# Optimization experiments

Hardware: AMD Instinct MI355X
Metric: run time of the kernel (lower is better)

## Reference

```python
import jax, jax.numpy as jnp
import numpy as np

LRELU_ALPHA = 0.2   # LeakyReLU negative slope (alpha init arg)
NEG_INF = -9e15     # masking constant used by standard GAT layers

B, N, NFEAT, NHID, NHEAD, NPRED = 16, 1024, 16, 32, 4, 12


def setup_inputs() -> dict:
    key = jax.random.key(0)
    ks = jax.random.split(key, 8)
    x = jax.random.normal(ks[0], (B, N, NFEAT), dtype=jnp.float32)
    adj = jax.random.randint(ks[1], (N, N), 0, 2, dtype=jnp.int32)
    s = 0.1
    W = jax.random.normal(ks[2], (NHEAD, NFEAT, NHID), dtype=jnp.float32) * s
    a_src = jax.random.normal(ks[3], (NHEAD, NHID), dtype=jnp.float32) * s
    a_dst = jax.random.normal(ks[4], (NHEAD, NHID), dtype=jnp.float32) * s
    W_out = jax.random.normal(ks[5], (NHEAD * NHID, NPRED), dtype=jnp.float32) * s
    a_out_src = jax.random.normal(ks[6], (NPRED,), dtype=jnp.float32) * s
    a_out_dst = jax.random.normal(ks[7], (NPRED,), dtype=jnp.float32) * s
    return {"x": x, "adj": adj, "W": W, "a_src": a_src, "a_dst": a_dst,
            "W_out": W_out, "a_out_src": a_out_src, "a_out_dst": a_out_dst}


def reference(x, adj, W, a_src, a_dst, W_out, a_out_src, a_out_dst):
    # Eval mode: all F.dropout calls are identity.
    mask = adj > 0  # [N, N], broadcast over batch (and heads)

    # --- multi-head GAT layer (concat=True), all heads vectorized ---
    Wh = jnp.einsum('bnf,hfk->bhnk', x, W)                 # [B,H,N,K]
    f_src = jnp.einsum('bhnk,hk->bhn', Wh, a_src)          # [B,H,N]
    f_dst = jnp.einsum('bhnk,hk->bhn', Wh, a_dst)
    e = jax.nn.leaky_relu(f_src[..., :, None] + f_dst[..., None, :], LRELU_ALPHA)
    attn = jax.nn.softmax(jnp.where(mask, e, NEG_INF), axis=-1)  # [B,H,N,N]
    h = jax.nn.elu(jnp.einsum('bhnm,bhmk->bhnk', attn, Wh))      # concat=True -> ELU
    b, H, n, k = h.shape
    h = jnp.transpose(h, (0, 2, 1, 3)).reshape(b, n, H * k)  # concat heads, dim=2

    # --- output GAT layer (concat=False) ---
    Wh2 = h @ W_out                                        # [B,N,npred]
    g_src = Wh2 @ a_out_src                                # [B,N]
    g_dst = Wh2 @ a_out_dst
    e2 = jax.nn.leaky_relu(g_src[:, :, None] + g_dst[:, None, :], LRELU_ALPHA)
    attn2 = jax.nn.softmax(jnp.where(mask, e2, NEG_INF), axis=-1)
    out = jax.nn.elu(jnp.einsum('bnm,bmp->bnp', attn2, Wh2))  # outer F.elu in STGAT
    return out.reshape(b, -1)                              # [B, N*npred]
```

## Files before the change

### kernel.cpp

```cpp
#include <hip/hip_runtime.h>
#include <cmath>

#define B_    16
#define N_    1024
#define NHID_ 32
#define NHEAD_ 4
#define NPRED_ 12
#define ALPHA 0.2f
#define LOG2E 1.442695041f

typedef __attribute__((ext_vector_type(8)))  short          short8;
typedef __attribute__((ext_vector_type(4)))  float          floatx4;
typedef __attribute__((ext_vector_type(2)))  float          float2v;
typedef __attribute__((ext_vector_type(4)))  unsigned       uintx4;
typedef __attribute__((ext_vector_type(4)))  unsigned short ushort4v;
typedef __attribute__((ext_vector_type(8)))  unsigned short ushort8v;

__device__ __forceinline__ float bs2f(unsigned short s) {
    return __uint_as_float(((unsigned)s) << 16);
}
__device__ __forceinline__ short f2bs(float f) {
    unsigned u = __float_as_uint(f);
    unsigned r = (u + 0x7fffu + ((u >> 16) & 1u)) >> 16;
    return (short)r;
}
__device__ __forceinline__ float ldin(const void* p, long i, int isbf) {
    if (isbf) return bs2f(((const unsigned short*)p)[i]);
    return ((const float*)p)[i];
}
__device__ __forceinline__ float fexp2(float x) {
#if __has_builtin(__builtin_amdgcn_exp2f)
    return __builtin_amdgcn_exp2f(x);
#else
    return __expf(x * 0.6931471805599453f);
#endif
}
__device__ __forceinline__ unsigned pk2t(unsigned u0, unsigned u1) {
#if __has_builtin(__builtin_amdgcn_perm)
    return __builtin_amdgcn_perm(u1, u0, 0x07060302u);
#else
    return (u0 >> 16) | (u1 & 0xffff0000u);
#endif
}
__device__ __forceinline__ float2v vmax2(float2v a, float2v b) {
#if __has_builtin(__builtin_elementwise_max)
    return __builtin_elementwise_max(a, b);
#else
    float2v r; r.x = fmaxf(a.x, b.x); r.y = fmaxf(a.y, b.y); return r;
#endif
}
__device__ __forceinline__ float2v vfma2(float2v a, float2v b, float2v c) {
#if __has_builtin(__builtin_elementwise_fma)
    return __builtin_elementwise_fma(a, b, c);
#else
    float2v r; r.x = __builtin_fmaf(a.x, b.x, c.x); r.y = __builtin_fmaf(a.y, b.y, c.y); return r;
#endif
}
__device__ __forceinline__ int detect_isbf(const unsigned short* xu) {
    int lane = threadIdx.x & 63;
    uint4 v = ((const uint4*)xu)[lane];
    unsigned wv[4] = {v.x, v.y, v.z, v.w};
    bool any = false;
#pragma unroll
    for (int i = 0; i < 4; ++i) {
        any |= (((wv[i] & 0xffffu) >> 7) & 0xffu) >= 160u;
        any |= (((wv[i] >> 16) >> 7) & 0xffu) >= 160u;
    }
    return __popcll(__ballot(any)) < 8;
}

__global__ __launch_bounds__(256) void k01_prep_wh(
    const unsigned short* __restrict__ xu, const int* __restrict__ adj,
    const void* __restrict__ x, const void* __restrict__ W,
    const void* __restrict__ a_src, const void* __restrict__ a_dst,
    unsigned short* __restrict__ bias,
    short* __restrict__ WhB, float* __restrict__ f_src, float* __restrict__ f_dst)
{
    int tid = threadIdx.x;
    if (blockIdx.x < 512) {
        int gid = blockIdx.x * 256 + tid;
        long base = (long)gid * 8;
        int4 a0 = *(const int4*)(adj + base);
        int4 a1 = *(const int4*)(adj + base + 4);
        uint4 wv;
        wv.x = (a0.x ? 0u : 0xFF80u) | (a0.y ? 0u : 0xFF800000u);
        wv.y = (a0.z ? 0u : 0xFF80u) | (a0.w ? 0u : 0xFF800000u);
        wv.z = (a1.x ? 0u : 0xFF80u) | (a1.y ? 0u : 0xFF800000u);
        wv.w = (a1.z ? 0u : 0xFF80u) | (a1.w ? 0u : 0xFF800000u);
        *(uint4*)(bias + base) = wv;
        return;
    }
    int isbf = detect_isbf(xu);
    __shared__ float Ws[16][32];
    __shared__ float xs[32][17];
    __shared__ float as_s[32], ad_s[32];
    __shared__ float Wa_s[16], Wad_s[16];
    int bid = blockIdx.x - 512;
    int bh = bid >> 5;
    int n0 = (bid & 31) * 32;
    int b  = bh >> 2, hh = bh & 3;

    if (!isbf) {
        const float* Wf = (const float*)W + hh * 512;
        if (tid < 128) {
            float4 v = *(const float4*)(Wf + tid * 4);
            int f = (tid * 4) >> 5, k = (tid * 4) & 31;
            Ws[f][k] = v.x; Ws[f][k+1] = v.y; Ws[f][k+2] = v.z; Ws[f][k+3] = v.w;
        }
        const float* xf = (const float*)x + ((long)(b * N_ + n0)) * 16;
        if (tid < 128) {
            float4 v = *(const float4*)(xf + tid * 4);
            int r = tid >> 2, f = (tid & 3) * 4;
            xs[r][f] = v.x; xs[r][f+1] = v.y; xs[r][f+2] = v.z; xs[r][f+3] = v.w;
        }
    } else {
        const unsigned short* Wb = (const unsigned short*)W + hh * 512;
        if (tid < 128) {
            ushort4v v = *(const ushort4v*)(Wb + tid * 4);
            int f = (tid * 4) >> 5, k = (tid * 4) & 31;
            Ws[f][k] = bs2f(v[0]); Ws[f][k+1] = bs2f(v[1]);
            Ws[f][k+2] = bs2f(v[2]); Ws[f][k+3] = bs2f(v[3]);
        }
        const unsigned short* xb = (const unsigned short*)x + ((long)(b * N_ + n0)) * 16;
        if (tid < 64) {
            ushort8v v = *(const ushort8v*)(xb + tid * 8);
            int r = tid >> 1, f = (tid & 1) * 8;
#pragma unroll
            for (int i = 0; i < 8; ++i) xs[r][f + i] = bs2f(v[i]);
        }
    }
    if (tid < 32) {
        as_s[tid] = ldin(a_src, hh * 32 + tid, isbf);
        ad_s[tid] = ldin(a_dst, hh * 32 + tid, isbf);
    }
    __syncthreads();

    if (tid < 32) {
        int f = tid & 15;
        const float* av = (tid < 16) ? as_s : ad_s;
        float s = 0.f;
#pragma unroll
        for (int kk = 0; kk < 32; ++kk) s += Ws[f][kk] * av[kk];
        ((tid < 16) ? Wa_s : Wad_s)[f] = s;
    }
    __syncthreads();

    if (tid < 32) {
        float fs = 0.f, fd = 0.f;
#pragma unroll
        for (int f = 0; f < 16; ++f) {
            fs += xs[tid][f] * Wa_s[f];
            fd += xs[tid][f] * Wad_s[f];
        }
        int n = n0 + tid;
        f_src[bh * N_ + n] = fs * LOG2E;
        f_dst[bh * N_ + n] = fd * LOG2E;
    }

    int k = tid & 31, rb = tid >> 5;
#pragma unroll
    for (int it = 0; it < 4; ++it) {
        int r = it * 8 + rb;
        float acc = 0.f;
#pragma unroll
        for (int f = 0; f < 16; ++f) acc += xs[r][f] * Ws[f][k];
        int n = n0 + r;
        int kstep = n >> 5, quad = (n >> 3) & 3, jj = n & 7;
        int t = k >> 4, l = quad * 16 + (k & 15);
        WhB[((((size_t)bh * 32 + kstep) * 2 + t) * 64 + l) * 8 + jj] = f2bs(acc);
    }
}

__global__ __launch_bounds__(256) void k2_attn1(
    const float* __restrict__ f_src, const float* __restrict__ f_dst,
    const unsigned short* __restrict__ bias, const short* __restrict__ WhB,
    unsigned short* __restrict__ h2)
{
    __shared__ float fdst_s[N_];
    __shared__ float wmax[4];
    __shared__ float Sh[2][2][16];
    __shared__ float xch[2][64][8];
    int bid = blockIdx.x;
    int xcd = bid & 7, j = bid >> 3;
    int bh = j & 63;
    int tile = xcd + 8 * (j >> 6);
    int tid = threadIdx.x;
    int w = tid >> 6, lane = tid & 63;
    int rh = w & 1, ch = w >> 1;

    float lmax = -INFINITY;
    for (int idx = tid; idx < N_; idx += 256) {
        float v = f_dst[bh * N_ + idx];
        fdst_s[idx] = v;
        lmax = fmaxf(lmax, v);
    }
#pragma unroll
    for (int m = 32; m; m >>= 1) lmax = fmaxf(lmax, __shfl_xor(lmax, m, 64));
    if (lane == 0) wmax[w] = lmax;
    __syncthreads();
    float maxfd = fmaxf(fmaxf(wmax[0], wmax[1]), fmaxf(wmax[2], wmax[3]));

    int i0 = tile * 32 + rh * 16;
    int r = lane & 15, q = lane >> 4;

    float fsr = f_src[bh * N_ + i0 + r];
    float Mv = fsr + maxfd;
    float M = fmaxf(Mv, ALPHA * Mv);
    float2v a1v; a1v.x = fsr - M;          a1v.y = a1v.x;
    float2v a2v; a2v.x = ALPHA * fsr - M;  a2v.y = a2v.x;
    float2v alv; alv.x = ALPHA;            alv.y = ALPHA;
    float2v s2 = {};

    floatx4 acc0 = {}, acc1 = {};
    const unsigned short* brow = bias + (size_t)(i0 + r) * N_ + ch * 512 + q * 8;
    const float* fdp = fdst_s + ch * 512 + q * 8;

    uint4  bu_n = *(const uint4*)(brow);
    float4 fa_n = *(const float4*)(fdp);
    float4 fb_n = *(const float4*)(fdp + 4);

#pragma unroll 4
    for (int kk = 0; kk < 16; ++kk) {
        uint4 bu = bu_n; float4 fda = fa_n; float4 fdb = fb_n;
        if (kk < 15) {
            bu_n = *(const uint4*)(brow + (kk + 1) * 32);
            fa_n = *(const float4*)(fdp + (kk + 1) * 32);
            fb_n = *(const float4*)(fdp + (kk + 1) * 32 + 4);
        }
        unsigned bw[4] = {bu.x, bu.y, bu.z, bu.w};
        float fdx[8] = {fda.x, fda.y, fda.z, fda.w, fdb.x, fdb.y, fdb.z, fdb.w};
        unsigned dpk[4];
#pragma unroll
        for (int p = 0; p < 4; ++p) {
            float2v fd2; fd2.x = fdx[2 * p]; fd2.y = fdx[2 * p + 1];
            float2v b2;  b2.x = __uint_as_float(bw[p] << 16);
                         b2.y = __uint_as_float(bw[p] & 0xffff0000u);
            float2v t1 = a1v + fd2;
            float2v t2 = vfma2(alv, fd2, a2v);
            float2v arg = vmax2(t1, t2) + b2;
            float2v pv; pv.x = fexp2(arg.x); pv.y = fexp2(arg.y);
            s2 += pv;
            dpk[p] = pk2t(__float_as_uint(pv.x), __float_as_uint(pv.y));
        }
        uintx4 du; du[0] = dpk[0]; du[1] = dpk[1]; du[2] = dpk[2]; du[3] = dpk[3];
        short8 afr = __builtin_bit_cast(short8, du);
        const short* bbase = WhB + ((((size_t)bh * 32 + ch * 16 + kk) * 2) * 64 + lane) * 8;
        short8 bfr0 = *(const short8*)(bbase);
        short8 bfr1 = *(const short8*)(bbase + 512);
        acc0 = __builtin_amdgcn_mfma_f32_16x16x32_bf16(afr, bfr0, acc0, 0, 0, 0);
        acc1 = __builtin_amdgcn_mfma_f32_16x16x32_bf16(afr, bfr1, acc1, 0, 0, 0);
    }

    float s = s2.x + s2.y;
    s += __shfl_xor(s, 16, 64);
    s += __shfl_xor(s, 32, 64);
    if (lane < 16) Sh[rh][ch][lane] = s;
    if (ch == 1) {
#pragma unroll
        for (int i = 0; i < 4; ++i) {
            xch[rh][lane][i]     = acc0[i];
            xch[rh][lane][4 + i] = acc1[i];
        }
    }
    __syncthreads();
    if (ch == 0) {
#pragma unroll
        for (int i = 0; i < 4; ++i) {
            acc0[i] += xch[rh][lane][i];
            acc1[i] += xch[rh][lane][4 + i];
        }
        int bb = bh >> 2, head = bh & 3;
#pragma unroll
        for (int reg = 0; reg < 4; ++reg) {
            int row = q * 4 + reg;
            float rsv = 1.f / (Sh[rh][0][row] + Sh[rh][1][row]);
            unsigned short* hrow = &h2[((size_t)(bb * N_ + i0 + row)) * 128 + head * 32];
            float v0 = acc0[reg] * rsv;
            v0 = v0 > 0.f ? v0 : expm1f(v0);
            hrow[r]      = (unsigned short)f2bs(v0);
            float v1 = acc1[reg] * rsv;
            v1 = v1 > 0.f ? v1 : expm1f(v1);
            hrow[16 + r] = (unsigned short)f2bs(v1);
        }
    }
}

__global__ __launch_bounds__(256) void k3_out_proj(
    const unsigned short* __restrict__ xu,
    const unsigned short* __restrict__ h2, const void* __restrict__ W_out,
    const void* __restrict__ a_out_src, const void* __restrict__ a_out_dst,
    short* __restrict__ Wh2B, float* __restrict__ g_src, float* __restrict__ g_dst)
{
    int isbf = detect_isbf(xu);
    __shared__ float WoT[16][132];
    __shared__ float hs[16][132];
    __shared__ float aos[16], aod[16];
    int bid = blockIdx.x;
    int b = bid >> 6;
    int n0 = (bid & 63) * 16;
    int tid = threadIdx.x;

    if (!isbf) {
        const float* Wf = (const float*)W_out;
        for (int idx = tid; idx < 384; idx += 256) {
            float4 v = *(const float4*)(Wf + idx * 4);
            float vv[4] = {v.x, v.y, v.z, v.w};
#pragma unroll
            for (int i = 0; i < 4; ++i) {
                int e = idx * 4 + i;
                WoT[e % NPRED_][e / NPRED_] = vv[i];
            }
        }
    } else {
        const unsigned short* Wb = (const unsigned short*)W_out;
        for (int idx = tid; idx < 192; idx += 256) {
            ushort8v v = *(const ushort8v*)(Wb + idx * 8);
#pragma unroll
            for (int i = 0; i < 8; ++i) {
                int e = idx * 8 + i;
                WoT[e % NPRED_][e / NPRED_] = bs2f(v[i]);
            }
        }
    }
    if (tid < 128) {
#pragma unroll
        for (int p = NPRED_; p < 16; ++p) WoT[p][tid] = 0.f;
    }
    if (tid < 16) {
        aos[tid] = (tid < NPRED_) ? ldin(a_out_src, tid, isbf) : 0.f;
        aod[tid] = (tid < NPRED_) ? ldin(a_out_dst, tid, isbf) : 0.f;
    }
    {
        ushort8v v = *(const ushort8v*)(h2 + ((size_t)(b * N_ + n0 + (tid >> 4))) * 128 + (tid & 15) * 8);
        int r = tid >> 4, c8 = (tid & 15) * 8;
#pragma unroll
        for (int i = 0; i < 8; ++i) hs[r][c8 + i] = bs2f(v[i]);
    }
    __syncthreads();

    int r = tid >> 4, p = tid & 15;
    float acc = 0.f;
#pragma unroll 8
    for (int c4 = 0; c4 < 128; c4 += 4) {
        float4 hv = *(const float4*)&hs[r][c4];
        float4 wv = *(const float4*)&WoT[p][c4];
        acc += hv.x * wv.x + hv.y * wv.y + hv.z * wv.z + hv.w * wv.w;
    }

    float t1 = acc * aos[p], t2 = acc * aod[p];
#pragma unroll
    for (int m = 8; m; m >>= 1) {
        t1 += __shfl_xor(t1, m, 64);
        t2 += __shfl_xor(t2, m, 64);
    }
    int n = n0 + r;
    if (p == 0) {
        g_src[b * N_ + n] = t1 * LOG2E;
        g_dst[b * N_ + n] = t2 * LOG2E;
    }
    int kstep = n >> 5, quad = (n >> 3) & 3, jj = n & 7;
    short val = (p == 15) ? (short)0x3F80 : f2bs(acc);
    Wh2B[(((size_t)b * 32 + kstep) * 64 + quad * 16 + p) * 8 + jj] = val;
}

__global__ __launch_bounds__(256) void k4_attn2(
    const unsigned short* __restrict__ xu,
    const float* __restrict__ g_src, const float* __restrict__ g_dst,
    const unsigned short* __restrict__ bias, const short* __restrict__ Wh2B,
    void* __restrict__ out)
{
    int isbf = detect_isbf(xu);
    __shared__ float gdst_s[N_];
    __shared__ float wmax[4];
    __shared__ float xch[3][64][4];
    int bid = blockIdx.x;
    int xcd = bid & 7, j = bid >> 3;
    int b = j & 15;
    int tile = xcd + 8 * (j >> 4);
    int tid = threadIdx.x;
    int ch = tid >> 6, lane = tid & 63;

    float lmax = -INFINITY;
    for (int idx = tid; idx < N_; idx += 256) {
        float v = g_dst[b * N_ + idx];
        gdst_s[idx] = v;
        lmax = fmaxf(lmax, v);
    }
#pragma unroll
    for (int m = 32; m; m >>= 1) lmax = fmaxf(lmax, __shfl_xor(lmax, m, 64));
    if (lane == 0) wmax[ch] = lmax;
    __syncthreads();
    float maxgd = fmaxf(fmaxf(wmax[0], wmax[1]), fmaxf(wmax[2], wmax[3]));

    int i0 = tile * 16;
    int r = lane & 15, q = lane >> 4;

    float gsr = g_src[b * N_ + i0 + r];
    float Mv = gsr + maxgd;
    float M = fmaxf(Mv, ALPHA * Mv);
    float2v a1v; a1v.x = gsr - M;          a1v.y = a1v.x;
    float2v a2v; a2v.x = ALPHA * gsr - M;  a2v.y = a2v.x;
    float2v alv; alv.x = ALPHA;            alv.y = ALPHA;

    floatx4 acc = {};
    const unsigned short* brow = bias + (size_t)(i0 + r) * N_ + ch * 256 + q * 8;
    const float* fdp = gdst_s + ch * 256 + q * 8;

    uint4  bu_n = *(const uint4*)(brow);
    float4 fa_n = *(const float4*)(fdp);
    float4 fb_n = *(const float4*)(fdp + 4);

#pragma unroll 4
    for (int kk = 0; kk < 8; ++kk) {
        uint4 bu = bu_n; float4 fda = fa_n; float4 fdb = fb_n;
        if (kk < 7) {
            bu_n = *(const uint4*)(brow + (kk + 1) * 32);
            fa_n = *(const float4*)(fdp + (kk + 1) * 32);
            fb_n = *(const float4*)(fdp + (kk + 1) * 32 + 4);
        }
        unsigned bw[4] = {bu.x, bu.y, bu.z, bu.w};
        float fdx[8] = {fda.x, fda.y, fda.z, fda.w, fdb.x, fdb.y, fdb.z, fdb.w};
        unsigned dpk[4];
#pragma unroll
        for (int p = 0; p < 4; ++p) {
            float2v fd2; fd2.x = fdx[2 * p]; fd2.y = fdx[2 * p + 1];
            float2v b2;  b2.x = __uint_as_float(bw[p] << 16);
                         b2.y = __uint_as_float(bw[p] & 0xffff0000u);
            float2v t1 = a1v + fd2;
            float2v t2 = vfma2(alv, fd2, a2v);
            float2v arg = vmax2(t1, t2) + b2;
            float2v pv; pv.x = fexp2(arg.x); pv.y = fexp2(arg.y);
            dpk[p] = pk2t(__float_as_uint(pv.x), __float_as_uint(pv.y));
        }
        uintx4 du; du[0] = dpk[0]; du[1] = dpk[1]; du[2] = dpk[2]; du[3] = dpk[3];
        short8 afr = __builtin_bit_cast(short8, du);
        short8 bfr = *(const short8*)(Wh2B + (((size_t)b * 32 + ch * 8 + kk) * 64 + lane) * 8);
        acc = __builtin_amdgcn_mfma_f32_16x16x32_bf16(afr, bfr, acc, 0, 0, 0);
    }

    if (ch != 0) {
#pragma unroll
        for (int i = 0; i < 4; ++i) xch[ch - 1][lane][i] = acc[i];
    }
    __syncthreads();
    if (ch == 0) {
#pragma unroll
        for (int t = 0; t < 3; ++t)
#pragma unroll
            for (int i = 0; i < 4; ++i) acc[i] += xch[t][lane][i];
        int srclane = (lane & 48) + 15;
#pragma unroll
        for (int reg = 0; reg < 4; ++reg) {
            int row = q * 4 + reg;
            float Srow = __shfl(acc[reg], srclane, 64);
            float v = acc[reg] / Srow;
            float o = v > 0.f ? v : expm1f(v);
            if (r < NPRED_) {
                size_t idx = (size_t)b * (N_ * NPRED_) + (size_t)(i0 + row) * NPRED_ + r;
                if (isbf) ((unsigned short*)out)[idx] = (unsigned short)f2bs(o);
                else      ((float*)out)[idx] = o;
            }
        }
    }
}

extern "C" void kernel_launch(void* const* d_in, const int* in_sizes, int n_in,
                              void* d_out, int out_size, void* d_ws, size_t ws_size,
                              hipStream_t stream)
{
    (void)in_sizes; (void)n_in; (void)out_size; (void)ws_size;
    const void* x      = d_in[0];
    const int*  adj    = (const int*)d_in[1];
    const void* W      = d_in[2];
    const void* a_src  = d_in[3];
    const void* a_dst  = d_in[4];
    const void* W_out  = d_in[5];
    const void* a_osrc = d_in[6];
    const void* a_odst = d_in[7];
    const unsigned short* xu = (const unsigned short*)x;

    char* ws = (char*)d_ws;
    short* WhB   = (short*)(ws);
    float* f_src = (float*)(ws + (4 << 20));
    float* f_dst = (float*)(ws + (4 << 20) + (256 << 10));
    unsigned short* h2 = (unsigned short*)(ws + (4 << 20) + (512 << 10));
    short* Wh2B  = (short*)(ws + (12 << 20) + (512 << 10));
    float* g_src = (float*)(ws + (13 << 20));
    float* g_dst = (float*)(ws + (13 << 20) + (64 << 10));
    unsigned short* bias = (unsigned short*)(ws + (14 << 20));

    hipLaunchKernelGGL(k01_prep_wh, dim3(2560), dim3(256), 0, stream,
                       xu, adj, x, W, a_src, a_dst, bias, WhB, f_src, f_dst);
    hipLaunchKernelGGL(k2_attn1,    dim3(2048), dim3(256), 0, stream,
                       f_src, f_dst, bias, WhB, h2);
    hipLaunchKernelGGL(k3_out_proj, dim3(1024), dim3(256), 0, stream,
                       xu, h2, W_out, a_osrc, a_odst, Wh2B, g_src, g_dst);
    hipLaunchKernelGGL(k4_attn2,    dim3(1024), dim3(256), 0, stream,
                       xu, g_src, g_dst, bias, Wh2B, d_out);
}
```

Measured before the change: 120.0 us.

## Stage bias tile in padded LDS and split attention K-range across four waves

Both attention kernels now cooperatively copy the 16-row bias tile into a padded shared-memory buffer with coalesced 16-byte loads, instead of each lane streaming its own strided global bias reads. k2 is restructured so each block handles 16 rows with four waves splitting the key dimension (a 4-way reduction of partial sums and accumulators), and the grid doubles to cover it. The Wh B-fragment loads are now software-prefetched one iteration ahead instead of the bias loads. This adds about 33KB of LDS per block, which may reduce occupancy, and adds a larger cross-wave reduction.

```diff
diff --git a/kernel.cpp b/kernel.cpp
--- a/kernel.cpp
+++ b/kernel.cpp
@@ -8,11 +8,13 @@
 #define NPRED_ 12
 #define ALPHA 0.2f
 #define LOG2E 1.442695041f
+#define BP    1044
 
 typedef __attribute__((ext_vector_type(8)))  short          short8;
 typedef __attribute__((ext_vector_type(4)))  float          floatx4;
 typedef __attribute__((ext_vector_type(2)))  float          float2v;
 typedef __attribute__((ext_vector_type(4)))  unsigned       uintx4;
+typedef __attribute__((ext_vector_type(2)))  unsigned       uintx2;
 typedef __attribute__((ext_vector_type(4)))  unsigned short ushort4v;
 typedef __attribute__((ext_vector_type(8)))  unsigned short ushort8v;
 
@@ -177,16 +179,17 @@
     unsigned short* __restrict__ h2)
 {
     __shared__ float fdst_s[N_];
+    __shared__ __align__(16) unsigned short bias_s[16 * BP];
     __shared__ float wmax[4];
-    __shared__ float Sh[2][2][16];
-    __shared__ float xch[2][64][8];
+    __shared__ float Sh[4][16];
+    __shared__ float xch[3][64][8];
     int bid = blockIdx.x;
     int xcd = bid & 7, j = bid >> 3;
     int bh = j & 63;
     int tile = xcd + 8 * (j >> 6);
     int tid = threadIdx.x;
-    int w = tid >> 6, lane = tid & 63;
-    int rh = w & 1, ch = w >> 1;
+    int ch = tid >> 6, lane = tid & 63;
+    int i0 = tile * 16;
 
     float lmax = -INFINITY;
     for (int idx = tid; idx < N_; idx += 256) {
@@ -196,11 +199,23 @@
     }
 #pragma unroll
     for (int m = 32; m; m >>= 1) lmax = fmaxf(lmax, __shfl_xor(lmax, m, 64));
-    if (lane == 0) wmax[w] = lmax;
+    if (lane == 0) wmax[ch] = lmax;
+
+    {
+        const unsigned short* gsrc = bias + (size_t)i0 * N_;
+#pragma unroll
+        for (int it = 0; it < 8; ++it) {
+            int e = (it * 256 + tid) * 8;
+            ushort8v v = *(const ushort8v*)(gsrc + e);
+            int rr = e >> 10, cc = e & 1023;
+            unsigned short* d = &bias_s[rr * BP + cc];
+            *(ushort4v*)d = __builtin_shufflevector(v, v, 0, 1, 2, 3);
+            *(ushort4v*)(d + 4) = __builtin_shufflevector(v, v, 4, 5, 6, 7);
+        }
+    }
     __syncthreads();
     float maxfd = fmaxf(fmaxf(wmax[0], wmax[1]), fmaxf(wmax[2], wmax[3]));
 
-    int i0 = tile * 32 + rh * 16;
     int r = lane & 15, q = lane >> 4;
 
     float fsr = f_src[bh * N_ + i0 + r];
@@ -212,22 +227,27 @@
     float2v s2 = {};
 
     floatx4 acc0 = {}, acc1 = {};
-    const unsigned short* brow = bias + (size_t)(i0 + r) * N_ + ch * 512 + q * 8;
-    const float* fdp = fdst_s + ch * 512 + q * 8;
-
-    uint4  bu_n = *(const uint4*)(brow);
-    float4 fa_n = *(const float4*)(fdp);
-    float4 fb_n = *(const float4*)(fdp + 4);
-
-#pragma unroll 4
-    for (int kk = 0; kk < 16; ++kk) {
-        uint4 bu = bu_n; float4 fda = fa_n; float4 fdb = fb_n;
-        if (kk < 15) {
-            bu_n = *(const uint4*)(brow + (kk + 1) * 32);
-            fa_n = *(const float4*)(fdp + (kk + 1) * 32);
-            fb_n = *(const float4*)(fdp + (kk + 1) * 32 + 4);
-        }
-        unsigned bw[4] = {bu.x, bu.y, bu.z, bu.w};
+    const unsigned short* bls = bias_s + r * BP + ch * 256 + q * 8;
+    const float* fdp = fdst_s + ch * 256 + q * 8;
+    const short* wb = WhB + ((((size_t)bh * 32 + ch * 8) * 2) * 64 + lane) * 8;
+
+    short8 w0_n = *(const short8*)(wb);
+    short8 w1_n = *(const short8*)(wb + 512);
+
+#pragma unroll
+    for (int kk = 0; kk < 8; ++kk) {
+        short8 bfr0 = w0_n, bfr1 = w1_n;
+        if (kk < 7) {
+            w0_n = *(const short8*)(wb + (kk + 1) * 1024);
+            w1_n = *(const short8*)(wb + (kk + 1) * 1024 + 512);
+        }
+        ushort4v blo = *(const ushort4v*)(bls + kk * 32);
+        ushort4v bhi = *(const ushort4v*)(bls + kk * 32 + 4);
+        uintx2 u0 = __builtin_bit_cast(uintx2, blo);
+        uintx2 u1 = __builtin_bit_cast(uintx2, bhi);
+        unsigned bw[4] = {u0[0], u0[1], u1[0], u1[1]};
+        float4 fda = *(const float4*)(fdp + kk * 32);
+        float4 fdb = *(const float4*)(fdp + kk * 32 + 4);
         float fdx[8] = {fda.x, fda.y, fda.z, fda.w, fdb.x, fdb.y, fdb.z, fdb.w};
         unsigned dpk[4];
 #pragma unroll
@@ -244,9 +264,6 @@
         }
         uintx4 du; du[0] = dpk[0]; du[1] = dpk[1]; du[2] = dpk[2]; du[3] = dpk[3];
         short8 afr = __builtin_bit_cast(short8, du);
-        const short* bbase = WhB + ((((size_t)bh * 32 + ch * 16 + kk) * 2) * 64 + lane) * 8;
-        short8 bfr0 = *(const short8*)(bbase);
-        short8 bfr1 = *(const short8*)(bbase + 512);
         acc0 = __builtin_amdgcn_mfma_f32_16x16x32_bf16(afr, bfr0, acc0, 0, 0, 0);
         acc1 = __builtin_amdgcn_mfma_f32_16x16x32_bf16(afr, bfr1, acc1, 0, 0, 0);
     }
@@ -254,26 +271,28 @@
     float s = s2.x + s2.y;
     s += __shfl_xor(s, 16, 64);
     s += __shfl_xor(s, 32, 64);
-    if (lane < 16) Sh[rh][ch][lane] = s;
-    if (ch == 1) {
+    if (lane < 16) Sh[ch][lane] = s;
+    if (ch != 0) {
 #pragma unroll
         for (int i = 0; i < 4; ++i) {
-            xch[rh][lane][i]     = acc0[i];
-            xch[rh][lane][4 + i] = acc1[i];
+            xch[ch - 1][lane][i]     = acc0[i];
+            xch[ch - 1][lane][4 + i] = acc1[i];
         }
     }
     __syncthreads();
     if (ch == 0) {
 #pragma unroll
-        for (int i = 0; i < 4; ++i) {
-            acc0[i] += xch[rh][lane][i];
-            acc1[i] += xch[rh][lane][4 + i];
-        }
+        for (int t = 0; t < 3; ++t)
+#pragma unroll
+            for (int i = 0; i < 4; ++i) {
+                acc0[i] += xch[t][lane][i];
+                acc1[i] += xch[t][lane][4 + i];
+            }
         int bb = bh >> 2, head = bh & 3;
 #pragma unroll
         for (int reg = 0; reg < 4; ++reg) {
             int row = q * 4 + reg;
-            float rsv = 1.f / (Sh[rh][0][row] + Sh[rh][1][row]);
+            float rsv = 1.f / (Sh[0][row] + Sh[1][row] + Sh[2][row] + Sh[3][row]);
             unsigned short* hrow = &h2[((size_t)(bb * N_ + i0 + row)) * 128 + head * 32];
             float v0 = acc0[reg] * rsv;
             v0 = v0 > 0.f ? v0 : expm1f(v0);
@@ -371,6 +390,7 @@
 {
     int isbf = detect_isbf(xu);
     __shared__ float gdst_s[N_];
+    __shared__ __align__(16) unsigned short bias_s[16 * BP];
     __shared__ float wmax[4];
     __shared__ float xch[3][64][4];
     int bid = blockIdx.x;
@@ -379,6 +399,7 @@
     int tile = xcd + 8 * (j >> 4);
     int tid = threadIdx.x;
     int ch = tid >> 6, lane = tid & 63;
+    int i0 = tile * 16;
 
     float lmax = -INFINITY;
     for (int idx = tid; idx < N_; idx += 256) {
@@ -389,10 +410,22 @@
 #pragma unroll
     for (int m = 32; m; m >>= 1) lmax = fmaxf(lmax, __shfl_xor(lmax, m, 64));
     if (lane == 0) wmax[ch] = lmax;
+
+    {
+        const unsigned short* gsrc = bias + (size_t)i0 * N_;
+#pragma unroll
+        for (int it = 0; it < 8; ++it) {
+            int e = (it * 256 + tid) * 8;
+            ushort8v v = *(const ushort8v*)(gsrc + e);
+            int rr = e >> 10, cc = e & 1023;
+            unsigned short* d = &bias_s[rr * BP + cc];
+            *(ushort4v*)d = __builtin_shufflevector(v, v, 0, 1, 2, 3);
+            *(ushort4v*)(d + 4) = __builtin_shufflevector(v, v, 4, 5, 6, 7);
+        }
+    }
     __syncthreads();
     float maxgd = fmaxf(fmaxf(wmax[0], wmax[1]), fmaxf(wmax[2], wmax[3]));
 
-    int i0 = tile * 16;
     int r = lane & 15, q = lane >> 4;
 
     float gsr = g_src[b * N_ + i0 + r];
@@ -403,22 +436,23 @@
     float2v alv; alv.x = ALPHA;            alv.y = ALPHA;
 
     floatx4 acc = {};
-    const unsigned short* brow = bias + (size_t)(i0 + r) * N_ + ch * 256 + q * 8;
+    const unsigned short* bls = bias_s + r * BP + ch * 256 + q * 8;
     const float* fdp = gdst_s + ch * 256 + q * 8;
-
-    uint4  bu_n = *(const uint4*)(brow);
-    float4 fa_n = *(const float4*)(fdp);
-    float4 fb_n = *(const float4*)(fdp + 4);
-
-#pragma unroll 4
+    const short* wb = Wh2B + (((size_t)b * 32 + ch * 8) * 64 + lane) * 8;
+
+    short8 wf_n = *(const short8*)(wb);
+
+#pragma unroll
     for (int kk = 0; kk < 8; ++kk) {
-        uint4 bu = bu_n; float4 fda = fa_n; float4 fdb = fb_n;
-        if (kk < 7) {
-            bu_n = *(const uint4*)(brow + (kk + 1) * 32);
-            fa_n = *(const float4*)(fdp + (kk + 1) * 32);
-            fb_n = *(const float4*)(fdp + (kk + 1) * 32 + 4);
-        }
-        unsigned bw[4] = {bu.x, bu.y, bu.z, bu.w};
+        short8 bfr = wf_n;
+        if (kk < 7) wf_n = *(const short8*)(wb + (kk + 1) * 512);
+        ushort4v blo = *(const ushort4v*)(bls + kk * 32);
+        ushort4v bhi = *(const ushort4v*)(bls + kk * 32 + 4);
+        uintx2 u0 = __builtin_bit_cast(uintx2, blo);
+        uintx2 u1 = __builtin_bit_cast(uintx2, bhi);
+        unsigned bw[4] = {u0[0], u0[1], u1[0], u1[1]};
+        float4 fda = *(const float4*)(fdp + kk * 32);
+        float4 fdb = *(const float4*)(fdp + kk * 32 + 4);
         float fdx[8] = {fda.x, fda.y, fda.z, fda.w, fdb.x, fdb.y, fdb.z, fdb.w};
         unsigned dpk[4];
 #pragma unroll
@@ -434,7 +468,6 @@
         }
         uintx4 du; du[0] = dpk[0]; du[1] = dpk[1]; du[2] = dpk[2]; du[3] = dpk[3];
         short8 afr = __builtin_bit_cast(short8, du);
-        short8 bfr = *(const short8*)(Wh2B + (((size_t)b * 32 + ch * 8 + kk) * 64 + lane) * 8);
         acc = __builtin_amdgcn_mfma_f32_16x16x32_bf16(afr, bfr, acc, 0, 0, 0);
     }
 
@@ -491,7 +524,7 @@
 
     hipLaunchKernelGGL(k01_prep_wh, dim3(2560), dim3(256), 0, stream,
                        xu, adj, x, W, a_src, a_dst, bias, WhB, f_src, f_dst);
-    hipLaunchKernelGGL(k2_attn1,    dim3(2048), dim3(256), 0, stream,
+    hipLaunchKernelGGL(k2_attn1,    dim3(4096), dim3(256), 0, stream,
                        f_src, f_dst, bias, WhB, h2);
     hipLaunchKernelGGL(k3_out_proj, dim3(1024), dim3(256), 0, stream,
                        xu, h2, W_out, a_osrc, a_odst, Wh2B, g_src, g_dst);
```

Measured after the change: 129.0 us. 7.5% more time.

## Give each wave a full key range in attn1 and prefetch MFMA B fragments

Applied to the files above, without the earlier changes.

The first attention kernel now has each of its four waves own 16 query rows across all 1024 keys, so a block covers 64 rows. This drops the split-K cross-wave reduction through shared memory and the block barrier, and halves the grid. Both attention kernels now software-prefetch the Wh B-fragments from global memory one iteration ahead and read the f_dst values from LDS on demand instead of prefetching them. In exchange, each wave runs a longer serial loop and there are fewer blocks to hide latency, while register pressure shifts from the LDS prefetch to the global prefetch.

```diff
diff --git a/kernel.cpp b/kernel.cpp
--- a/kernel.cpp
+++ b/kernel.cpp
@@ -178,15 +178,13 @@
 {
     __shared__ float fdst_s[N_];
     __shared__ float wmax[4];
-    __shared__ float Sh[2][2][16];
-    __shared__ float xch[2][64][8];
+    __shared__ float Sh[4][16];
     int bid = blockIdx.x;
     int xcd = bid & 7, j = bid >> 3;
     int bh = j & 63;
     int tile = xcd + 8 * (j >> 6);
     int tid = threadIdx.x;
     int w = tid >> 6, lane = tid & 63;
-    int rh = w & 1, ch = w >> 1;
 
     float lmax = -INFINITY;
     for (int idx = tid; idx < N_; idx += 256) {
@@ -200,7 +198,7 @@
     __syncthreads();
     float maxfd = fmaxf(fmaxf(wmax[0], wmax[1]), fmaxf(wmax[2], wmax[3]));
 
-    int i0 = tile * 32 + rh * 16;
+    int i0 = tile * 64 + w * 16;
     int r = lane & 15, q = lane >> 4;
 
     float fsr = f_src[bh * N_ + i0 + r];
@@ -212,21 +210,25 @@
     float2v s2 = {};
 
     floatx4 acc0 = {}, acc1 = {};
-    const unsigned short* brow = bias + (size_t)(i0 + r) * N_ + ch * 512 + q * 8;
-    const float* fdp = fdst_s + ch * 512 + q * 8;
+    const unsigned short* brow = bias + (size_t)(i0 + r) * N_ + q * 8;
+    const float* fdp = fdst_s + q * 8;
+    const short* wb = WhB + (((size_t)bh * 64) * 64 + lane) * 8;
 
     uint4  bu_n = *(const uint4*)(brow);
-    float4 fa_n = *(const float4*)(fdp);
-    float4 fb_n = *(const float4*)(fdp + 4);
+    short8 w0_n = *(const short8*)(wb);
+    short8 w1_n = *(const short8*)(wb + 512);
 
 #pragma unroll 4
-    for (int kk = 0; kk < 16; ++kk) {
-        uint4 bu = bu_n; float4 fda = fa_n; float4 fdb = fb_n;
-        if (kk < 15) {
+    for (int kk = 0; kk < 32; ++kk) {
+        uint4 bu = bu_n;
+        short8 bfr0 = w0_n, bfr1 = w1_n;
+        if (kk < 31) {
             bu_n = *(const uint4*)(brow + (kk + 1) * 32);
-            fa_n = *(const float4*)(fdp + (kk + 1) * 32);
-            fb_n = *(const float4*)(fdp + (kk + 1) * 32 + 4);
-        }
+            w0_n = *(const short8*)(wb + (kk + 1) * 1024);
+            w1_n = *(const short8*)(wb + (kk + 1) * 1024 + 512);
+        }
+        float4 fda = *(const float4*)(fdp + kk * 32);
+        float4 fdb = *(const float4*)(fdp + kk * 32 + 4);
         unsigned bw[4] = {bu.x, bu.y, bu.z, bu.w};
         float fdx[8] = {fda.x, fda.y, fda.z, fda.w, fdb.x, fdb.y, fdb.z, fdb.w};
         unsigned dpk[4];
@@ -244,9 +246,6 @@
         }
         uintx4 du; du[0] = dpk[0]; du[1] = dpk[1]; du[2] = dpk[2]; du[3] = dpk[3];
         short8 afr = __builtin_bit_cast(short8, du);
-        const short* bbase = WhB + ((((size_t)bh * 32 + ch * 16 + kk) * 2) * 64 + lane) * 8;
-        short8 bfr0 = *(const short8*)(bbase);
-        short8 bfr1 = *(const short8*)(bbase + 512);
         acc0 = __builtin_amdgcn_mfma_f32_16x16x32_bf16(afr, bfr0, acc0, 0, 0, 0);
         acc1 = __builtin_amdgcn_mfma_f32_16x16x32_bf16(afr, bfr1, acc1, 0, 0, 0);
     }
@@ -254,34 +253,21 @@
     float s = s2.x + s2.y;
     s += __shfl_xor(s, 16, 64);
     s += __shfl_xor(s, 32, 64);
-    if (lane < 16) Sh[rh][ch][lane] = s;
-    if (ch == 1) {
-#pragma unroll
-        for (int i = 0; i < 4; ++i) {
-            xch[rh][lane][i]     = acc0[i];
-            xch[rh][lane][4 + i] = acc1[i];
-        }
-    }
-    __syncthreads();
-    if (ch == 0) {
-#pragma unroll
-        for (int i = 0; i < 4; ++i) {
-            acc0[i] += xch[rh][lane][i];
-            acc1[i] += xch[rh][lane][4 + i];
-        }
-        int bb = bh >> 2, head = bh & 3;
-#pragma unroll
-        for (int reg = 0; reg < 4; ++reg) {
-            int row = q * 4 + reg;
-            float rsv = 1.f / (Sh[rh][0][row] + Sh[rh][1][row]);
-            unsigned short* hrow = &h2[((size_t)(bb * N_ + i0 + row)) * 128 + head * 32];
-            float v0 = acc0[reg] * rsv;
-            v0 = v0 > 0.f ? v0 : expm1f(v0);
-            hrow[r]      = (unsigned short)f2bs(v0);
-            float v1 = acc1[reg] * rsv;
-            v1 = v1 > 0.f ? v1 : expm1f(v1);
-            hrow[16 + r] = (unsigned short)f2bs(v1);
-        }
+    if (lane < 16) Sh[w][lane] = s;
+    __builtin_amdgcn_wave_barrier();
+
+    int bb = bh >> 2, head = bh & 3;
+#pragma unroll
+    for (int reg = 0; reg < 4; ++reg) {
+        int row = q * 4 + reg;
+        float rsv = 1.f / Sh[w][row];
+        unsigned short* hrow = &h2[((size_t)(bb * N_ + i0 + row)) * 128 + head * 32];
+        float v0 = acc0[reg] * rsv;
+        v0 = v0 > 0.f ? v0 : expm1f(v0);
+        hrow[r]      = (unsigned short)f2bs(v0);
+        float v1 = acc1[reg] * rsv;
+        v1 = v1 > 0.f ? v1 : expm1f(v1);
+        hrow[16 + r] = (unsigned short)f2bs(v1);
     }
 }
 
@@ -405,19 +391,21 @@
     floatx4 acc = {};
     const unsigned short* brow = bias + (size_t)(i0 + r) * N_ + ch * 256 + q * 8;
     const float* fdp = gdst_s + ch * 256 + q * 8;
+    const short* wb = Wh2B + (((size_t)b * 32 + ch * 8) * 64 + lane) * 8;
 
     uint4  bu_n = *(const uint4*)(brow);
-    float4 fa_n = *(const float4*)(fdp);
-    float4 fb_n = *(const float4*)(fdp + 4);
+    short8 wf_n = *(const short8*)(wb);
 
 #pragma unroll 4
     for (int kk = 0; kk < 8; ++kk) {
-        uint4 bu = bu_n; float4 fda = fa_n; float4 fdb = fb_n;
+        uint4 bu = bu_n;
+        short8 bfr = wf_n;
         if (kk < 7) {
             bu_n = *(const uint4*)(brow + (kk + 1) * 32);
-            fa_n = *(const float4*)(fdp + (kk + 1) * 32);
-            fb_n = *(const float4*)(fdp + (kk + 1) * 32 + 4);
-        }
+            wf_n = *(const short8*)(wb + (kk + 1) * 512);
+        }
+        float4 fda = *(const float4*)(fdp + kk * 32);
+        float4 fdb = *(const float4*)(fdp + kk * 32 + 4);
         unsigned bw[4] = {bu.x, bu.y, bu.z, bu.w};
         float fdx[8] = {fda.x, fda.y, fda.z, fda.w, fdb.x, fdb.y, fdb.z, fdb.w};
         unsigned dpk[4];
@@ -434,7 +422,6 @@
         }
         uintx4 du; du[0] = dpk[0]; du[1] = dpk[1]; du[2] = dpk[2]; du[3] = dpk[3];
         short8 afr = __builtin_bit_cast(short8, du);
-        short8 bfr = *(const short8*)(Wh2B + (((size_t)b * 32 + ch * 8 + kk) * 64 + lane) * 8);
         acc = __builtin_amdgcn_mfma_f32_16x16x32_bf16(afr, bfr, acc, 0, 0, 0);
     }
 
@@ -491,7 +478,7 @@
 
     hipLaunchKernelGGL(k01_prep_wh, dim3(2560), dim3(256), 0, stream,
                        xu, adj, x, W, a_src, a_dst, bias, WhB, f_src, f_dst);
-    hipLaunchKernelGGL(k2_attn1,    dim3(2048), dim3(256), 0, stream,
+    hipLaunchKernelGGL(k2_attn1,    dim3(1024), dim3(256), 0, stream,
                        f_src, f_dst, bias, WhB, h2);
     hipLaunchKernelGGL(k3_out_proj, dim3(1024), dim3(256), 0, stream,
                        xu, h2, W_out, a_osrc, a_odst, Wh2B, g_src, g_dst);
```

Result: no change. 121.1 us (+0.9%).
